# Optimization experiments

Measured on AMD Instinct MI355X. Metric: run time of the kernel, lower is better.

## Reference

```python
import jax, jax.numpy as jnp
import numpy as np

N_NODES = 100000
N_EDGES = 1000000
KEY_DIM = 128
VAL_DIM = 64


def setup_inputs() -> dict:
    key = jax.random.key(0)
    k0, k1, k2, k3, k4, k5 = jax.random.split(key, 6)
    triples = jax.random.randint(k0, (N_EDGES, 3), 0, N_NODES, dtype=jnp.int64)
    ent_feats = jax.random.normal(k1, (N_NODES, KEY_DIM), dtype=jnp.float32)
    att_feats = jax.random.normal(k2, (N_NODES, KEY_DIM), dtype=jnp.float32)
    val_feats = jax.random.normal(k3, (N_NODES, VAL_DIM), dtype=jnp.float32)
    # a: Linear(2*key_dim, 1) -> weight vector [2k], bias [1]
    a_w = jax.random.normal(k4, (2 * KEY_DIM,), dtype=jnp.float32) * (1.0 / np.sqrt(2 * KEY_DIM))
    a_b = jnp.zeros((1,), dtype=jnp.float32)
    W = jax.random.normal(k5, (KEY_DIM + VAL_DIM, KEY_DIM), dtype=jnp.float32) * (1.0 / np.sqrt(KEY_DIM + VAL_DIM))
    return {"attribute_triples": triples, "ent_feats": ent_feats,
            "att_feats": att_feats, "val_feats": val_feats,
            "a_w": a_w, "a_b": a_b, "W": W}


def reference(attribute_triples, ent_feats, att_feats, val_feats, a_w, a_b, W):
    N = ent_feats.shape[0]
    h = attribute_triples[:, 0]
    att = attribute_triples[:, 1]
    val = attribute_triples[:, 2]
    # edge attention score: a([e_h ; a_att]) -> leaky_relu -> exp
    e_h = ent_feats[h]            # [E, K]
    a_f = att_feats[att]          # [E, K]
    score = jnp.concatenate((e_h, a_f), axis=-1) @ a_w + a_b[0]   # [E]
    score = jnp.exp(jax.nn.leaky_relu(score, negative_slope=0.2))
    # segment softmax denominator per head node
    row_sum = jax.ops.segment_sum(score, h, num_segments=N)       # [N]
    attention_p = score / row_sum[h]                               # [E]
    # projected edge messages, weighted by attention, scattered to nodes
    av = jnp.concatenate((a_f, val_feats[val]), axis=-1) @ W       # [E, K]
    av = av * attention_p[:, None]
    to_feats = jax.ops.segment_sum(av, h, num_segments=N)          # [N, K]
    return jax.nn.elu(to_feats + ent_feats)
```

## Files before the change

### kernel.cpp

```cpp
#include <hip/hip_runtime.h>

#define N_NODES 100000
#define N_EDGES 1000000
#define CAP     40

typedef __attribute__((ext_vector_type(8))) short short8;
typedef __attribute__((ext_vector_type(4))) short short4v;
typedef __attribute__((ext_vector_type(4))) float float4_t;

__device__ __forceinline__ unsigned short f_to_bf(float f) {
    union { float f; unsigned int i; } c; c.f = f;
    unsigned int x = c.i;
    unsigned int r = x + 0x7fffu + ((x >> 16) & 1u);
    return (unsigned short)(r >> 16);
}
__device__ __forceinline__ float bf_to_f(unsigned short u) {
    union { unsigned int i; float f; } c; c.i = ((unsigned int)u) << 16; return c.f;
}
__device__ __forceinline__ unsigned int pack2(float x, float y) {
    return (unsigned int)f_to_bf(x) | ((unsigned int)f_to_bf(y) << 16);
}
__device__ __forceinline__ unsigned short f_to_h(float f) {
    union { float f; unsigned int i; } c; c.f = f;
    unsigned int i = c.i;
    unsigned int e = ((i >> 23) & 0xffu) - 112u;
    unsigned int m = i & 0x7fffffu;
    unsigned int r = (e << 10) | (m >> 13);
    r += (m >> 12) & 1u;
    return (unsigned short)r;
}
__device__ __forceinline__ float h_to_f(unsigned short h) {
    union { unsigned int i; float f; } c;
    c.i = (((unsigned int)(h & 0x7fffu)) << 13) + 0x38000000u;
    return c.f;
}
__device__ __forceinline__ int clampi(int x) {
    return x < 0 ? 0 : (x >= N_NODES ? N_NODES - 1 : x);
}

__global__ __launch_bounds__(256)
void k_node_scores(const float* __restrict__ ent,
                   const float* __restrict__ attf,
                   const float* __restrict__ valf,
                   const float* __restrict__ aw,
                   float* __restrict__ s_ent, float* __restrict__ s_att,
                   unsigned short* __restrict__ attb,
                   unsigned short* __restrict__ valb) {
    int node = (int)((blockIdx.x * blockDim.x + threadIdx.x) >> 6);
    int lane = threadIdx.x & 63;
    if (node >= N_NODES) return;
    const float2* aw2 = (const float2*)aw;
    float2 we = aw2[lane];
    float2 wa = aw2[64 + lane];
    float2 e2 = ((const float2*)ent)[(size_t)node * 64 + lane];
    float2 a2 = ((const float2*)attf)[(size_t)node * 64 + lane];
    if (attb) ((unsigned int*)attb)[(size_t)node * 64 + lane] = pack2(a2.x, a2.y);
    if (valb) valb[(size_t)node * 64 + lane] = f_to_bf(valf[(size_t)node * 64 + lane]);
    float se = e2.x * we.x + e2.y * we.y;
    float sa = a2.x * wa.x + a2.y * wa.y;
#pragma unroll
    for (int off = 32; off >= 1; off >>= 1) {
        se += __shfl_xor(se, off, 64);
        sa += __shfl_xor(sa, off, 64);
    }
    if (lane == 0) { s_ent[node] = se; s_att[node] = sa; }
}

__global__ __launch_bounds__(256)
void k_prepW(const float* __restrict__ W, unsigned short* __restrict__ Wt) {
    int i = (int)(blockIdx.x * blockDim.x + threadIdx.x);
    if (i >= 192 * 128) return;
    int c = i / 192, k = i - c * 192;
    Wt[i] = f_to_bf(W[k * 128 + c]);
}

__global__ __launch_bounds__(256)
void k_place(const int* __restrict__ tri,
             const float* __restrict__ s_ent, const float* __restrict__ s_att,
             const float* __restrict__ abp,
             int* __restrict__ cursor, unsigned long long* __restrict__ edges) {
    int t = (int)(blockIdx.x * blockDim.x + threadIdx.x);
    if (t >= N_EDGES / 4) return;
    const int4* t4 = (const int4*)tri;
    int4 w0 = t4[3 * t], w1 = t4[3 * t + 1], w2 = t4[3 * t + 2];
    int hs[4] = {w0.x, w0.w, w1.z, w2.y};
    int as[4] = {w0.y, w1.x, w1.w, w2.z};
    int vs[4] = {w0.z, w1.y, w2.x, w2.w};
    float ab = abp[0];
#pragma unroll
    for (int i = 0; i < 4; ++i) {
        int h = clampi(hs[i]), a = clampi(as[i]), v = clampi(vs[i]);
        float s = s_ent[h] + s_att[a] + ab;
        s = s > 0.f ? s : 0.2f * s;
        float sc = __expf(s);
        int slot = atomicAdd(&cursor[h], 1);
        if (slot < CAP) {
            unsigned long long pk = (unsigned long long)(unsigned)a
                                  | ((unsigned long long)(unsigned)v << 17)
                                  | ((unsigned long long)f_to_h(sc) << 34);
            edges[(size_t)h * CAP + slot] = pk;
        }
    }
}

template<int ABF, int VBF>
__global__ __launch_bounds__(256)
void k_fused(const int* __restrict__ cursor, const unsigned long long* __restrict__ edges,
             const float* __restrict__ attf, const float* __restrict__ valf,
             const unsigned short* __restrict__ attb, const unsigned short* __restrict__ valb,
             const unsigned short* __restrict__ Wt, const float* __restrict__ ent,
             float* __restrict__ out) {
    __shared__ unsigned short Gl[16][200];
    int w = threadIdx.x >> 6, lane = threadIdx.x & 63;
    int grp = lane >> 4, l = lane & 15;
    int base = (int)blockIdx.x * 16;

    for (int nn = 0; nn < 4; ++nn) {
        int node = base + w * 4 + nn;
        int cnt = cursor[node]; if (cnt > CAP) cnt = CAP;
        size_t beg = (size_t)node * CAP;
        float aa[8] = {0.f, 0.f, 0.f, 0.f, 0.f, 0.f, 0.f, 0.f};
        float av[4] = {0.f, 0.f, 0.f, 0.f};
        float rsum = 0.f;
        for (int j = grp; j < cnt; j += 4) {
            unsigned long long ed = edges[beg + j];
            int a = (int)(ed & 0x1FFFFu);
            int v = (int)((ed >> 17) & 0x1FFFFu);
            float sc = h_to_f((unsigned short)(ed >> 34));
            rsum += sc;
            if (ABF) {
                short8 af = *(const short8*)(attb + (size_t)a * 128 + l * 8);
#pragma unroll
                for (int q = 0; q < 8; ++q) aa[q] += sc * bf_to_f((unsigned short)af[q]);
            } else {
                const float4_t* ap = (const float4_t*)(attf + (size_t)a * 128);
                float4_t f0 = ap[l], f1 = ap[16 + l];
#pragma unroll
                for (int q = 0; q < 4; ++q) { aa[q] += sc * f0[q]; aa[4 + q] += sc * f1[q]; }
            }
            if (VBF) {
                short4v vf = *(const short4v*)(valb + (size_t)v * 64 + l * 4);
#pragma unroll
                for (int q = 0; q < 4; ++q) av[q] += sc * bf_to_f((unsigned short)vf[q]);
            } else {
                float4_t fv = ((const float4_t*)(valf + (size_t)v * 64))[l];
#pragma unroll
                for (int q = 0; q < 4; ++q) av[q] += sc * fv[q];
            }
        }
#pragma unroll
        for (int q = 0; q < 8; ++q) {
            aa[q] += __shfl_xor(aa[q], 16, 64);
            aa[q] += __shfl_xor(aa[q], 32, 64);
        }
#pragma unroll
        for (int q = 0; q < 4; ++q) {
            av[q] += __shfl_xor(av[q], 16, 64);
            av[q] += __shfl_xor(av[q], 32, 64);
        }
        rsum += __shfl_xor(rsum, 16, 64);
        rsum += __shfl_xor(rsum, 32, 64);
        if (grp == 0) {
            float inv = rsum > 0.f ? 1.f / rsum : 0.f;
            unsigned short* gp = &Gl[w * 4 + nn][0];
            if (ABF) {
                uint4 pk;
                pk.x = pack2(aa[0] * inv, aa[1] * inv);
                pk.y = pack2(aa[2] * inv, aa[3] * inv);
                pk.z = pack2(aa[4] * inv, aa[5] * inv);
                pk.w = pack2(aa[6] * inv, aa[7] * inv);
                *(uint4*)(gp + l * 8) = pk;
            } else {
                uint2 p0; p0.x = pack2(aa[0] * inv, aa[1] * inv); p0.y = pack2(aa[2] * inv, aa[3] * inv);
                *(uint2*)(gp + l * 4) = p0;
                uint2 p1; p1.x = pack2(aa[4] * inv, aa[5] * inv); p1.y = pack2(aa[6] * inv, aa[7] * inv);
                *(uint2*)(gp + 64 + l * 4) = p1;
            }
            uint2 pv; pv.x = pack2(av[0] * inv, av[1] * inv); pv.y = pack2(av[2] * inv, av[3] * inv);
            *(uint2*)(gp + 128 + l * 4) = pv;
        }
    }
    __syncthreads();

    int quad = grp, mn = l;
    float4_t acc0 = {0.f, 0.f, 0.f, 0.f}, acc1 = {0.f, 0.f, 0.f, 0.f};
#pragma unroll
    for (int kt = 0; kt < 6; ++kt) {
        short8 afr = *(const short8*)(&Gl[mn][quad * 8 + kt * 32]);
        short8 b0 = *(const short8*)(Wt + (size_t)((w * 2 + 0) * 16 + mn) * 192 + quad * 8 + kt * 32);
        short8 b1 = *(const short8*)(Wt + (size_t)((w * 2 + 1) * 16 + mn) * 192 + quad * 8 + kt * 32);
        acc0 = __builtin_amdgcn_mfma_f32_16x16x32_bf16(afr, b0, acc0, 0, 0, 0);
        acc1 = __builtin_amdgcn_mfma_f32_16x16x32_bf16(afr, b1, acc1, 0, 0, 0);
    }
#pragma unroll
    for (int cti = 0; cti < 2; ++cti) {
        float4_t acc = cti ? acc1 : acc0;
        int col = (w * 2 + cti) * 16 + mn;
#pragma unroll
        for (int r = 0; r < 4; ++r) {
            int node = base + quad * 4 + r;
            float x = acc[r] + ent[(size_t)node * 128 + col];
            out[(size_t)node * 128 + col] = x > 0.f ? x : expm1f(x);
        }
    }
}

extern "C" void kernel_launch(void* const* d_in, const int* in_sizes, int n_in,
                              void* d_out, int out_size, void* d_ws, size_t ws_size,
                              hipStream_t stream) {
    const int*   tri  = (const int*)d_in[0];
    const float* ent  = (const float*)d_in[1];
    const float* attf = (const float*)d_in[2];
    const float* valf = (const float*)d_in[3];
    const float* aw   = (const float*)d_in[4];
    const float* ab   = (const float*)d_in[5];
    const float* W    = (const float*)d_in[6];
    float* out = (float*)d_out;

    char* ws = (char*)d_ws;
    size_t off = 0;
    int*   cursor = (int*)(ws + off);   off += (size_t)N_NODES * 4;
    float* s_ent  = (float*)(ws + off); off += (size_t)N_NODES * 4;
    float* s_att  = (float*)(ws + off); off += (size_t)N_NODES * 4;
    unsigned short* Wt = (unsigned short*)(ws + off); off += 192 * 128 * 2;
    unsigned long long* edges = (unsigned long long*)(ws + off);
    off += (size_t)N_NODES * CAP * 8;
    unsigned short* attb = (unsigned short*)(ws + off); off += (size_t)N_NODES * 128 * 2;
    size_t need_a = off;
    unsigned short* valb = (unsigned short*)(ws + off); off += (size_t)N_NODES * 64 * 2;
    size_t need_av = off;
    int abf = ws_size >= need_a;
    int vbf = ws_size >= need_av;

    hipMemsetAsync(cursor, 0, (size_t)N_NODES * 4, stream);

    k_node_scores<<<N_NODES / 4, 256, 0, stream>>>(ent, attf, valf, aw, s_ent, s_att,
                                                   abf ? attb : (unsigned short*)nullptr,
                                                   vbf ? valb : (unsigned short*)nullptr);
    k_prepW<<<(192 * 128 + 255) / 256, 256, 0, stream>>>(W, Wt);
    k_place<<<(N_EDGES / 4 + 255) / 256, 256, 0, stream>>>(tri, s_ent, s_att, ab, cursor, edges);
    if (abf && vbf)
        k_fused<1, 1><<<N_NODES / 16, 256, 0, stream>>>(cursor, edges, attf, valf, attb, valb, Wt, ent, out);
    else if (abf)
        k_fused<1, 0><<<N_NODES / 16, 256, 0, stream>>>(cursor, edges, attf, valf, attb, valb, Wt, ent, out);
    else
        k_fused<0, 0><<<N_NODES / 16, 256, 0, stream>>>(cursor, edges, attf, valf, attb, valb, Wt, ent, out);
}
```

Measured before the change: 342.8 us.

## Add bf16 fused kernel with register-cached edges and masked dual-edge gathers

Introduces a specialized bf16 aggregation kernel that loads each warp's edge lists into registers once and distributes them via shuffles, processes two edges per iteration with branch-free masked gathers pointing to a zeroed sentinel row, and uses packed float2 FMAs. Sentinel rows are appended to the bf16 feature buffers and cleared with extra memsets. The placement kernel is changed from four edges per thread with vectorized int4 loads to one edge per thread. This aims to increase memory-level parallelism in the gather phase at the cost of extra wasted loads on padding edges.

```diff
diff --git a/kernel.cpp b/kernel.cpp
--- a/kernel.cpp
+++ b/kernel.cpp
@@ -7,6 +7,8 @@
 typedef __attribute__((ext_vector_type(8))) short short8;
 typedef __attribute__((ext_vector_type(4))) short short4v;
 typedef __attribute__((ext_vector_type(4))) float float4_t;
+typedef __attribute__((ext_vector_type(2))) float floatx2;
+typedef unsigned long long ull;
 
 __device__ __forceinline__ unsigned short f_to_bf(float f) {
     union { float f; unsigned int i; } c; c.f = f;
@@ -33,6 +35,11 @@
     union { unsigned int i; float f; } c;
     c.i = (((unsigned int)(h & 0x7fffu)) << 13) + 0x38000000u;
     return c.f;
+}
+__device__ __forceinline__ floatx2 up2(unsigned int u) {
+    union { unsigned int i; float f; } lo, hi;
+    lo.i = u << 16; hi.i = u & 0xffff0000u;
+    floatx2 r; r.x = lo.f; r.y = hi.f; return r;
 }
 __device__ __forceinline__ int clampi(int x) {
     return x < 0 ? 0 : (x >= N_NODES ? N_NODES - 1 : x);
@@ -78,34 +85,124 @@
 void k_place(const int* __restrict__ tri,
              const float* __restrict__ s_ent, const float* __restrict__ s_att,
              const float* __restrict__ abp,
-             int* __restrict__ cursor, unsigned long long* __restrict__ edges) {
-    int t = (int)(blockIdx.x * blockDim.x + threadIdx.x);
-    if (t >= N_EDGES / 4) return;
-    const int4* t4 = (const int4*)tri;
-    int4 w0 = t4[3 * t], w1 = t4[3 * t + 1], w2 = t4[3 * t + 2];
-    int hs[4] = {w0.x, w0.w, w1.z, w2.y};
-    int as[4] = {w0.y, w1.x, w1.w, w2.z};
-    int vs[4] = {w0.z, w1.y, w2.x, w2.w};
-    float ab = abp[0];
-#pragma unroll
-    for (int i = 0; i < 4; ++i) {
-        int h = clampi(hs[i]), a = clampi(as[i]), v = clampi(vs[i]);
-        float s = s_ent[h] + s_att[a] + ab;
-        s = s > 0.f ? s : 0.2f * s;
-        float sc = __expf(s);
-        int slot = atomicAdd(&cursor[h], 1);
-        if (slot < CAP) {
-            unsigned long long pk = (unsigned long long)(unsigned)a
-                                  | ((unsigned long long)(unsigned)v << 17)
-                                  | ((unsigned long long)f_to_h(sc) << 34);
-            edges[(size_t)h * CAP + slot] = pk;
+             int* __restrict__ cursor, ull* __restrict__ edges) {
+    int e = (int)(blockIdx.x * blockDim.x + threadIdx.x);
+    if (e >= N_EDGES) return;
+    int h = clampi(tri[3 * e]);
+    int a = clampi(tri[3 * e + 1]);
+    int v = clampi(tri[3 * e + 2]);
+    float s = s_ent[h] + s_att[a] + abp[0];
+    s = s > 0.f ? s : 0.2f * s;
+    float sc = __expf(s);
+    int slot = atomicAdd(&cursor[h], 1);
+    if (slot < CAP) {
+        ull pk = (ull)(unsigned)a | ((ull)(unsigned)v << 17) | ((ull)f_to_h(sc) << 34);
+        edges[(size_t)h * CAP + slot] = pk;
+    }
+}
+
+__global__ __launch_bounds__(256)
+void k_fused_bf(const int* __restrict__ cursor, const ull* __restrict__ edges,
+                const unsigned short* __restrict__ attb, const unsigned short* __restrict__ valb,
+                const unsigned short* __restrict__ Wt, const float* __restrict__ ent,
+                float* __restrict__ out) {
+    __shared__ unsigned short Gl[16][200];
+    int w = threadIdx.x >> 6, lane = threadIdx.x & 63;
+    int grp = lane >> 4, l = lane & 15;
+    int base = (int)blockIdx.x * 16;
+    int nb = base + w * 4;
+
+    int4 cnt4 = *(const int4*)(cursor + nb);
+    int li = lane < CAP ? lane : CAP - 1;
+    ull edr[4];
+#pragma unroll
+    for (int nn = 0; nn < 4; ++nn) edr[nn] = edges[(size_t)(nb + nn) * CAP + li];
+
+    const char* ab = (const char*)attb;
+    const char* vb = (const char*)valb;
+
+#pragma unroll
+    for (int nn = 0; nn < 4; ++nn) {
+        int cnt = (nn == 0) ? cnt4.x : (nn == 1) ? cnt4.y : (nn == 2) ? cnt4.z : cnt4.w;
+        cnt = cnt > CAP ? CAP : cnt;
+        ull edreg = edr[nn];
+        floatx2 aa0 = {0.f, 0.f}, aa1 = {0.f, 0.f}, aa2 = {0.f, 0.f}, aa3 = {0.f, 0.f};
+        floatx2 av0 = {0.f, 0.f}, av1 = {0.f, 0.f};
+        float rsum = 0.f;
+        int kmax = (cnt + 7) >> 3;
+        for (int k = 0; k < kmax; ++k) {
+            int j0 = grp + (k << 3), j1 = j0 + 4;
+            bool m0 = j0 < cnt, m1 = j1 < cnt;
+            ull e0 = __shfl(edreg, m0 ? j0 : 0, 64);
+            ull e1 = __shfl(edreg, m1 ? j1 : 0, 64);
+            unsigned a0 = m0 ? (unsigned)(e0 & 0x1FFFFu) : (unsigned)N_NODES;
+            unsigned v0 = m0 ? (unsigned)((e0 >> 17) & 0x1FFFFu) : (unsigned)N_NODES;
+            float   sc0 = m0 ? h_to_f((unsigned short)(e0 >> 34)) : 0.f;
+            unsigned a1 = m1 ? (unsigned)(e1 & 0x1FFFFu) : (unsigned)N_NODES;
+            unsigned v1 = m1 ? (unsigned)((e1 >> 17) & 0x1FFFFu) : (unsigned)N_NODES;
+            float   sc1 = m1 ? h_to_f((unsigned short)(e1 >> 34)) : 0.f;
+            uint4 A0 = *(const uint4*)(ab + (a0 << 8) + (l << 4));
+            uint2 V0 = *(const uint2*)(vb + (v0 << 7) + (l << 3));
+            uint4 A1 = *(const uint4*)(ab + (a1 << 8) + (l << 4));
+            uint2 V1 = *(const uint2*)(vb + (v1 << 7) + (l << 3));
+            rsum += sc0 + sc1;
+            floatx2 s0; s0.x = sc0; s0.y = sc0;
+            floatx2 s1; s1.x = sc1; s1.y = sc1;
+            aa0 += s0 * up2(A0.x); aa1 += s0 * up2(A0.y);
+            aa2 += s0 * up2(A0.z); aa3 += s0 * up2(A0.w);
+            av0 += s0 * up2(V0.x); av1 += s0 * up2(V0.y);
+            aa0 += s1 * up2(A1.x); aa1 += s1 * up2(A1.y);
+            aa2 += s1 * up2(A1.z); aa3 += s1 * up2(A1.w);
+            av0 += s1 * up2(V1.x); av1 += s1 * up2(V1.y);
+        }
+#define RED2(x) x += __shfl_xor(x, 16, 64); x += __shfl_xor(x, 32, 64)
+        RED2(aa0.x); RED2(aa0.y); RED2(aa1.x); RED2(aa1.y);
+        RED2(aa2.x); RED2(aa2.y); RED2(aa3.x); RED2(aa3.y);
+        RED2(av0.x); RED2(av0.y); RED2(av1.x); RED2(av1.y);
+        RED2(rsum);
+#undef RED2
+        if (grp == 0) {
+            float inv = rsum > 0.f ? 1.f / rsum : 0.f;
+            unsigned short* gp = &Gl[w * 4 + nn][0];
+            uint4 pk;
+            pk.x = pack2(aa0.x * inv, aa0.y * inv);
+            pk.y = pack2(aa1.x * inv, aa1.y * inv);
+            pk.z = pack2(aa2.x * inv, aa2.y * inv);
+            pk.w = pack2(aa3.x * inv, aa3.y * inv);
+            *(uint4*)(gp + l * 8) = pk;
+            uint2 pv; pv.x = pack2(av0.x * inv, av0.y * inv);
+            pv.y = pack2(av1.x * inv, av1.y * inv);
+            *(uint2*)(gp + 128 + l * 4) = pv;
+        }
+    }
+    __syncthreads();
+
+    int quad = grp, mn = l;
+    float4_t acc0 = {0.f, 0.f, 0.f, 0.f}, acc1 = {0.f, 0.f, 0.f, 0.f};
+#pragma unroll
+    for (int kt = 0; kt < 6; ++kt) {
+        short8 afr = *(const short8*)(&Gl[mn][quad * 8 + kt * 32]);
+        short8 b0 = *(const short8*)(Wt + (size_t)((w * 2 + 0) * 16 + mn) * 192 + quad * 8 + kt * 32);
+        short8 b1 = *(const short8*)(Wt + (size_t)((w * 2 + 1) * 16 + mn) * 192 + quad * 8 + kt * 32);
+        acc0 = __builtin_amdgcn_mfma_f32_16x16x32_bf16(afr, b0, acc0, 0, 0, 0);
+        acc1 = __builtin_amdgcn_mfma_f32_16x16x32_bf16(afr, b1, acc1, 0, 0, 0);
+    }
+#pragma unroll
+    for (int cti = 0; cti < 2; ++cti) {
+        float4_t acc = cti ? acc1 : acc0;
+        int col = (w * 2 + cti) * 16 + mn;
+#pragma unroll
+        for (int r = 0; r < 4; ++r) {
+            int node = base + quad * 4 + r;
+            float x = acc[r] + ent[(size_t)node * 128 + col];
+            out[(size_t)node * 128 + col] = x > 0.f ? x : expm1f(x);
         }
     }
 }
 
 template<int ABF, int VBF>
 __global__ __launch_bounds__(256)
-void k_fused(const int* __restrict__ cursor, const unsigned long long* __restrict__ edges,
+void k_fused(const int* __restrict__ cursor, const ull* __restrict__ edges,
              const float* __restrict__ attf, const float* __restrict__ valf,
              const unsigned short* __restrict__ attb, const unsigned short* __restrict__ valb,
              const unsigned short* __restrict__ Wt, const float* __restrict__ ent,
@@ -123,7 +220,7 @@
         float av[4] = {0.f, 0.f, 0.f, 0.f};
         float rsum = 0.f;
         for (int j = grp; j < cnt; j += 4) {
-            unsigned long long ed = edges[beg + j];
+            ull ed = edges[beg + j];
             int a = (int)(ed & 0x1FFFFu);
             int v = (int)((ed >> 17) & 0x1FFFFu);
             float sc = h_to_f((unsigned short)(ed >> 34));
@@ -223,24 +320,27 @@
     float* s_ent  = (float*)(ws + off); off += (size_t)N_NODES * 4;
     float* s_att  = (float*)(ws + off); off += (size_t)N_NODES * 4;
     unsigned short* Wt = (unsigned short*)(ws + off); off += 192 * 128 * 2;
-    unsigned long long* edges = (unsigned long long*)(ws + off);
-    off += (size_t)N_NODES * CAP * 8;
-    unsigned short* attb = (unsigned short*)(ws + off); off += (size_t)N_NODES * 128 * 2;
+    ull* edges = (ull*)(ws + off);      off += (size_t)N_NODES * CAP * 8;
+    unsigned short* attb = (unsigned short*)(ws + off);
+    off += (size_t)(N_NODES + 1) * 128 * 2;
     size_t need_a = off;
-    unsigned short* valb = (unsigned short*)(ws + off); off += (size_t)N_NODES * 64 * 2;
+    unsigned short* valb = (unsigned short*)(ws + off);
+    off += (size_t)(N_NODES + 1) * 64 * 2;
     size_t need_av = off;
     int abf = ws_size >= need_a;
     int vbf = ws_size >= need_av;
 
     hipMemsetAsync(cursor, 0, (size_t)N_NODES * 4, stream);
+    if (abf) hipMemsetAsync(attb + (size_t)N_NODES * 128, 0, 256, stream);
+    if (vbf) hipMemsetAsync(valb + (size_t)N_NODES * 64, 0, 128, stream);
 
     k_node_scores<<<N_NODES / 4, 256, 0, stream>>>(ent, attf, valf, aw, s_ent, s_att,
                                                    abf ? attb : (unsigned short*)nullptr,
                                                    vbf ? valb : (unsigned short*)nullptr);
     k_prepW<<<(192 * 128 + 255) / 256, 256, 0, stream>>>(W, Wt);
-    k_place<<<(N_EDGES / 4 + 255) / 256, 256, 0, stream>>>(tri, s_ent, s_att, ab, cursor, edges);
+    k_place<<<(N_EDGES + 255) / 256, 256, 0, stream>>>(tri, s_ent, s_att, ab, cursor, edges);
     if (abf && vbf)
-        k_fused<1, 1><<<N_NODES / 16, 256, 0, stream>>>(cursor, edges, attf, valf, attb, valb, Wt, ent, out);
+        k_fused_bf<<<N_NODES / 16, 256, 0, stream>>>(cursor, edges, attb, valb, Wt, ent, out);
     else if (abf)
         k_fused<1, 0><<<N_NODES / 16, 256, 0, stream>>>(cursor, edges, attf, valf, attb, valb, Wt, ent, out);
     else
```

Result: faster. 332.0 us (-3.2%).
